# Kernel optimization log

Measured on AMD Instinct MI355X. Metric: run time of the kernel, lower is better.

Reference implementation:

```python
import jax, jax.numpy as jnp
import numpy as np

EPS = 1e-4
SLOPE = 0.01
NFFT = 512
HOP = 256
CH_IN = 8
CH_H = 64
FREQ = NFFT // 2 + 1
LEN = 48000
BATCH = 2


def hann(n):
    return (0.5 - 0.5 * jnp.cos(2.0 * np.pi * jnp.arange(n) / n)).astype(jnp.float32)


def stft(x):
    # x: (B, C, L) -> (B, 2, C, F, T)  (torch.stft: center=True, reflect pad, hann window)
    pad = NFFT // 2
    xp = jnp.pad(x, ((0, 0), (0, 0), (pad, pad)), mode='reflect')
    T = 1 + x.shape[-1] // HOP
    idx = jnp.arange(T)[:, None] * HOP + jnp.arange(NFFT)[None, :]
    frames = xp[..., idx] * hann(NFFT)            # (B, C, T, NFFT)
    sp = jnp.fft.rfft(frames, axis=-1)            # (B, C, T, F)
    sp = jnp.swapaxes(sp, -1, -2)                 # (B, C, F, T)
    return jnp.stack([sp.real, sp.imag], axis=1).astype(jnp.float32)


def istft(re, im, length):
    # re, im: (B, C, F, T) -> (B, C, length) via windowed overlap-add
    sp = jnp.swapaxes(re + 1j * im, -1, -2)       # (B, C, T, F)
    win = hann(NFFT)
    frames = jnp.fft.irfft(sp, n=NFFT, axis=-1) * win
    pad = NFFT // 2
    total = length + 2 * pad
    T = frames.shape[-2]
    idx = jnp.arange(T)[:, None] * HOP + jnp.arange(NFFT)[None, :]
    out = jnp.zeros(frames.shape[:-2] + (total,), frames.dtype).at[..., idx].add(frames)
    wsum = jnp.zeros((total,), frames.dtype).at[idx].add(jnp.broadcast_to(win ** 2, (T, NFFT)))
    return (out / jnp.maximum(wsum, 1e-11))[..., pad:pad + length]


def conv2d(x, w, b, padT=0):
    y = jax.lax.conv_general_dilated(x, w, (1, 1), ((0, 0), (padT, padT)),
                                     dimension_numbers=('NCHW', 'OIHW', 'NCHW'))
    return y + b[None, :, None, None]


def cconv(x, w, b, padT=0):
    # complex conv on x: (B,2,C,F,T); w: (2,O,C,kf,kt) = [W_real, W_imag]; b: (2,O)
    r = conv2d(x[:, 0], w[0], b[0], padT) - conv2d(x[:, 1], w[1], b[1], padT)
    i = conv2d(x[:, 1], w[0], b[0], padT) + conv2d(x[:, 0], w[1], b[1], padT)
    return jnp.stack([r, i], axis=1)


def modExp(x, m=5.0):
    em = float(np.exp(m))
    return jnp.where(x > m, (x - m) * em + em, jnp.exp(jnp.minimum(x, m)))


def cExp(t):
    e = modExp(t[:, 0]) - 1.0
    return jnp.stack([e * jnp.cos(t[:, 1] - 1.0), e * jnp.sin(t[:, 1] - 1.0)], axis=1)


def snap(x):
    x = jnp.where((x >= 0) & (x < EPS), EPS, x)
    return jnp.where((x < 0) & (x > -EPS), -EPS, x)


def cLog(t):
    re = snap(t[:, 0])
    im = snap(t[:, 1])
    real = jnp.log(jnp.sqrt(im ** 2 + re ** 2 + EPS ** 2) + 1.0)
    imag = jnp.arctan(im / re)
    return jnp.stack([real, imag], axis=1)


def cMul(a, b):
    r = a[:, 0] * b[:, 0] - a[:, 1] * b[:, 1]
    i = a[:, 0] * b[:, 1] + a[:, 1] * b[:, 0]
    return jnp.stack([r, i], axis=1)


def trelu(t, tr, b):
    nr = t[:, 0] * tr[0, 0] + t[:, 1] * tr[0, 1] + b[0]
    ni = t[:, 0] * tr[1, 0] + t[:, 1] * tr[1, 1] + b[1]
    return jnp.stack([jax.nn.leaky_relu(nr, SLOPE), jax.nn.leaky_relu(ni, SLOPE)], axis=1)


def tgate(t, tr, b):
    gr = jax.nn.sigmoid(t[:, 0] * tr[0, 0] + t[:, 1] * tr[0, 1] + b[0])
    gi = jax.nn.sigmoid(t[:, 0] * tr[1, 0] + t[:, 1] * tr[1, 1] + b[1])
    return gr * gi + (1.0 - gr) * (1.0 - gi)


def perm(t):
    return jnp.transpose(t, (0, 1, 3, 2, 4))


def lrelu(x):
    return jax.nn.leaky_relu(x, SLOPE)


def forward(mix, fs_w, fs_b, fr_w, fr_b, c1r_w, c1r_b, c1i_w, c1i_b, c1_w, c1_b,
            c2r_w, c2r_b, c2i_w, c2i_b, c2_w, c2_b, a1_t, a1_b, a2_t, a2_b,
            c3r_w, c3r_b, c3i_w, c3i_b, c3_w, c3_b, c4r_w, c4r_b, c4i_w, c4i_b,
            c4_w, c4_b, a3_t, a3_b, a4_t, a4_b, f1_w, f1_b, f2_w, f2_b,
            cw_w, cw_b, fg_t, fg_b):
    ts = perm(cconv(perm(stft(mix)), fs_w, fs_b))      # (B,2,C,F,T)
    # ---- branch 1 ----
    tl = cLog(ts)
    tl = jnp.stack([conv2d(tl[:, 0], c1r_w, c1r_b), conv2d(tl[:, 1], c1r_w, c1r_b)], 1)
    tl = jnp.stack([conv2d(lrelu(tl[:, 0]), c1i_w, c1i_b), conv2d(tl[:, 1], c1i_w, c1i_b)], 1)
    tl = trelu(cExp(tl), a1_t, a1_b)
    t = cconv(tl, c1_w, c1_b)
    tl = cLog(t)
    tl = jnp.stack([conv2d(tl[:, 0], c2r_w, c2r_b, 7), conv2d(tl[:, 1], c2r_w, c2r_b, 7)], 1)[..., :-7]
    tl = jnp.stack([conv2d(lrelu(tl[:, 0]), c2i_w, c2i_b, 7), conv2d(tl[:, 1], c2i_w, c2i_b, 7)], 1)[..., :-7]
    tl = cExp(tl)
    tl1 = tl
    tc = cconv(ts, c2_w, c2_b, 7)[..., :-7]
    t = trelu(cMul(tl, tc), a2_t, a2_b)
    t = cconv(t, f1_w, f1_b)
    td1 = jnp.sum(ts - t, axis=2, keepdims=True) / ts.shape[2]
    # ---- branch 2 ----
    tl = cLog(ts)
    tl = jnp.stack([conv2d(tl[:, 0], c3r_w, c3r_b), conv2d(tl[:, 1], c3r_w, c3r_b)], 1)
    tl = jnp.stack([conv2d(lrelu(tl[:, 0]), c3i_w, c3i_b), conv2d(tl[:, 1], c3i_w, c3i_b)], 1)
    tl = trelu(cExp(tl), a3_t, a3_b)
    t = cconv(tl, c3_w, c3_b)
    tl = cLog(t)
    tl = jnp.stack([conv2d(tl[:, 0], c4r_w, c4r_b, 7), conv2d(tl[:, 1], c4r_w, c4r_b, 7)], 1)[..., :-7]
    tl = jnp.stack([conv2d(lrelu(tl[:, 0]), c4i_w, c4i_b, 7), conv2d(tl[:, 1], c4i_w, c4i_b, 7)], 1)[..., :-7]
    tl = cExp(tl)
    tc = cconv(ts, c4_w, c4_b, 7)[..., :-7]
    t = trelu(cMul(tl, tc), a4_t, a4_b)
    td2 = cconv(t, f2_w, f2_b)                         # (B,2,1,F,T)
    # ---- fuse ----
    f = cconv(jnp.concatenate([tl1, tl], axis=2), cw_w, cw_b)
    f = tgate(f, fg_t, fg_b)[:, None]                  # (B,1,1,F,T)
    td = td1 * f + td2 * (1.0 - f)
    t = perm(cconv(perm(td), fr_w, fr_b))
    return istft(t[:, 0], t[:, 1], LEN)                # (B,1,LEN)


def setup_inputs() -> dict:
    ks = iter(jax.random.split(jax.random.key(0), 64))
    def rn(shape, s=0.05):
        return s * jax.random.normal(next(ks), shape, jnp.float32)
    F, C, H = FREQ, CH_IN, CH_H
    inp = {
        'mix': jax.random.normal(next(ks), (BATCH, C, LEN), jnp.float32),
        'fs_w': rn((2, F, F, 1, 1)), 'fs_b': rn((2, F), 0.01),
        'fr_w': rn((2, F, F, 1, 1)), 'fr_b': rn((2, F), 0.01),
        'c1r_w': rn((H, C, 1, 1)), 'c1r_b': rn((H,), 0.01),
        'c1i_w': rn((H, H, 1, 1)), 'c1i_b': rn((H,), 0.01),
        'c1_w': rn((2, H, H, 1, 1)), 'c1_b': rn((2, H), 0.01),
        'c2r_w': rn((H, H, 1, 8)), 'c2r_b': rn((H,), 0.01),
        'c2i_w': rn((H, H, 1, 8)), 'c2i_b': rn((H,), 0.01),
        'c2_w': rn((2, H, C, 1, 8)), 'c2_b': rn((2, H), 0.01),
        'a1_t': rn((2, 2, H, F, 1), 0.5), 'a1_b': rn((2, H, F, 1), 0.5),
        'a2_t': rn((2, 2, H, F, 1), 0.5), 'a2_b': rn((2, H, F, 1), 0.5),
        'c3r_w': rn((H, C, 1, 1)), 'c3r_b': rn((H,), 0.01),
        'c3i_w': rn((H, H, 1, 1)), 'c3i_b': rn((H,), 0.01),
        'c3_w': rn((2, H, H, 1, 1)), 'c3_b': rn((2, H), 0.01),
        'c4r_w': rn((H, H, 1, 8)), 'c4r_b': rn((H,), 0.01),
        'c4i_w': rn((H, H, 1, 8)), 'c4i_b': rn((H,), 0.01),
        'c4_w': rn((2, H, C, 1, 8)), 'c4_b': rn((2, H), 0.01),
        'a3_t': rn((2, 2, H, F, 1), 0.5), 'a3_b': rn((2, H, F, 1), 0.5),
        'a4_t': rn((2, 2, H, F, 1), 0.5), 'a4_b': rn((2, H, F, 1), 0.5),
        'f1_w': rn((2, C, H, 1, 1)), 'f1_b': rn((2, C), 0.01),
        'f2_w': rn((2, 1, H, 1, 1)), 'f2_b': rn((2, 1), 0.01),
        'cw_w': rn((2, 1, 2 * H, 1, 1)), 'cw_b': rn((2, 1), 0.01),
        'fg_t': rn((2, 2, 1, F, 1), 0.5), 'fg_b': rn((2, 1, F, 1), 0.5),
    }
    return inp


def reference(mix, fs_w, fs_b, fr_w, fr_b, c1r_w, c1r_b, c1i_w, c1i_b, c1_w, c1_b,
              c2r_w, c2r_b, c2i_w, c2i_b, c2_w, c2_b, a1_t, a1_b, a2_t, a2_b,
              c3r_w, c3r_b, c3i_w, c3i_b, c3_w, c3_b, c4r_w, c4r_b, c4i_w, c4i_b,
              c4_w, c4_b, a3_t, a3_b, a4_t, a4_b, f1_w, f1_b, f2_w, f2_b,
              cw_w, cw_b, fg_t, fg_b):
    return forward(mix, fs_w, fs_b, fr_w, fr_b, c1r_w, c1r_b, c1i_w, c1i_b, c1_w, c1_b,
                   c2r_w, c2r_b, c2i_w, c2i_b, c2_w, c2_b, a1_t, a1_b, a2_t, a2_b,
                   c3r_w, c3r_b, c3i_w, c3i_b, c3_w, c3_b, c4r_w, c4r_b, c4i_w, c4i_b,
                   c4_w, c4_b, a3_t, a3_b, a4_t, a4_b, f1_w, f1_b, f2_w, f2_b,
                   cw_w, cw_b, fg_t, fg_b)
```

## Files before the change

### kernel.cpp

```cpp
#include <hip/hip_runtime.h>
#include <math.h>

#define DEV __device__ __forceinline__

constexpr int B_   = 2;
constexpr int C_IN = 8;
constexpr int H_   = 64;
constexpr int F_   = 257;
constexpr int T_   = 188;
constexpr int TW   = 96;
constexpr int NFFT = 512;
constexpr int HOP  = 256;
constexpr int LEN  = 48000;
constexpr int PADL = 256;
constexpr int FT   = F_ * T_;
constexpr float EPSV  = 1e-4f;
constexpr float SLOPEV = 0.01f;
constexpr float PI2 = 6.283185307179586f;

typedef __attribute__((ext_vector_type(8))) short short8;
typedef __attribute__((ext_vector_type(4))) short short4v;
typedef __attribute__((ext_vector_type(4))) float float4v;

DEV float lrelu_f(float x) { return x > 0.f ? x : SLOPEV * x; }
DEV float snap_f(float x) {
  if (x >= 0.f && x < EPSV) return EPSV;
  if (x < 0.f && x > -EPSV) return -EPSV;
  return x;
}
DEV float modexp_f(float x) {
  const float em = 148.4131591025766f;
  return x > 5.f ? (x - 5.f) * em + em : expf(x);
}
DEV void cexp_f(float tr, float ti, float& er, float& ei) {
  float e = modexp_f(tr) - 1.f;
  float s, c;
  sincosf(ti - 1.f, &s, &c);
  er = e * c; ei = e * s;
}
DEV float sigmoid_f(float x) { return 1.f / (1.f + expf(-x)); }

DEV short f2bf(float x) {
  unsigned u = __float_as_uint(x);
  unsigned r = (u + 0x7fffu + ((u >> 16) & 1u)) >> 16;
  return (short)r;
}
DEV float bf2f(short h) {
  return __uint_as_float(((unsigned)(unsigned short)h) << 16);
}

__global__ void k_mixsplit(const float* __restrict__ x, short* __restrict__ hi,
                           short* __restrict__ lo) {
  int i = blockIdx.x * 256 + threadIdx.x;
  if (i >= B_ * C_IN * LEN / 4) return;
  float4v v = *(const float4v*)(x + (size_t)i * 4);
  short4v h, l;
  #pragma unroll
  for (int j = 0; j < 4; ++j) {
    h[j] = f2bf(v[j]);
    l[j] = f2bf(v[j] - bf2f(h[j]));
  }
  *(short4v*)(hi + (size_t)i * 4) = h;
  *(short4v*)(lo + (size_t)i * 4) = l;
}

__global__ __launch_bounds__(256) void k_mixdft(const float* __restrict__ W,
                                                short* __restrict__ wpk) {
  constexpr int MT = 33;
  __shared__ float wr_s[F_], wi_s[F_];
  int m = blockIdx.x;
  int k = blockIdx.y * 256 + threadIdx.x;
  int po = m >= F_;
  int fo = m - po * F_;
  if (m < 2 * F_) {
    for (int i = threadIdx.x; i < F_; i += 256) {
      wr_s[i] = W[fo * F_ + i];
      wi_s[i] = W[F_ * F_ + fo * F_ + i];
    }
  }
  __syncthreads();
  float val = 0.f;
  if (m < 2 * F_) {
    float sd, cd;
    sincosf((PI2 / NFFT) * k, &sd, &cd);
    float cs = 1.f, sn = 0.f;
    float ar = 0.f, ai = 0.f;
    for (int fi = 0; fi < F_; ++fi) {
      float wrv = wr_s[fi], wiv = wi_s[fi];
      ar += wrv * cs + wiv * sn;
      ai += wiv * cs - wrv * sn;
      float t2 = cs * cd - sn * sd;
      sn = sn * cd + cs * sd;
      cs = t2;
    }
    float win = 0.5f - 0.5f * cd;
    val = (po ? ai : ar) * win;
  }
  int mtg = m >> 4;
  int lane2 = ((k >> 3) & 3) * 16 + (m & 15);
  int s = k >> 5;
  int j = k & 7;
  short hi = f2bf(val);
  short lo = f2bf(val - bf2f(hi));
  wpk[(((0 * 16 + s) * MT + mtg) * 64 + lane2) * 8 + j] = hi;
  wpk[(((16 + s) * MT + mtg) * 64 + lane2) * 8 + j] = lo;
}

__global__ __launch_bounds__(256) void k_stftmix(
    const short* __restrict__ mhi, const short* __restrict__ mlo,
    const short* __restrict__ wpk, const float* __restrict__ bias,
    float* __restrict__ Y) {
  constexpr int PITCH = 136;
  constexpr int MT = 33;
  __shared__ short xs_hi[TW * PITCH];
  __shared__ short xs_lo[TW * PITCH];
  int mg = blockIdx.x;
  int bc = blockIdx.y;
  int b = bc >> 3, c = bc & 7;
  int t0 = blockIdx.z * TW;
  int tid = threadIdx.x;
  int lane = tid & 63;
  int wv = __builtin_amdgcn_readfirstlane(tid >> 6);
  int mh = wv >> 1;
  int tc = wv & 1;
  int q = lane >> 4;
  int n = lane & 15;
  int wbase = tc * 48;

  const short* mh_ = mhi + (size_t)(b * C_IN + c) * LEN;
  const short* ml_ = mlo + (size_t)(b * C_IN + c) * LEN;

  float4v acc[2][3];
  #pragma unroll
  for (int mt = 0; mt < 2; ++mt)
    #pragma unroll
    for (int nt = 0; nt < 3; ++nt) acc[mt][nt] = (float4v)(0.f);

  const short8* wp = (const short8*)wpk;
  for (int round = 0; round < 4; ++round) {
    if (round) __syncthreads();
    for (int i = tid; i < TW * 16; i += 256) {
      int tl = i >> 4, u = i & 15;
      int kk0 = u * 8;
      int t = t0 + tl;
      int g0 = t * HOP + round * 128 + kk0 - PADL;
      short8 h, l;
      if (t < T_ && g0 >= 0 && g0 + 7 < LEN) {
        h = *(const short8*)(mh_ + g0);
        l = *(const short8*)(ml_ + g0);
      } else {
        #pragma unroll
        for (int j = 0; j < 8; ++j) {
          short hv = 0, lv = 0;
          if (t < T_) {
            int g = g0 + j;
            if (g < 0) g = -g;
            if (g >= LEN) g = 2 * LEN - 2 - g;
            hv = mh_[g]; lv = ml_[g];
          }
          h[j] = hv; l[j] = lv;
        }
      }
      *(short8*)&xs_hi[tl * PITCH + kk0] = h;
      *(short8*)&xs_lo[tl * PITCH + kk0] = l;
    }
    __syncthreads();
    #pragma unroll
    for (int s2 = 0; s2 < 4; ++s2) {
      int s = round * 4 + s2;
      short8 Bh[3], Bl[3];
      #pragma unroll
      for (int nt = 0; nt < 3; ++nt) {
        int off = (wbase + nt * 16 + n) * PITCH + s2 * 32 + q * 8;
        Bh[nt] = *(const short8*)&xs_hi[off];
        Bl[nt] = *(const short8*)&xs_lo[off];
      }
      #pragma unroll
      for (int mt = 0; mt < 2; ++mt) {
        int mtg = mg * 4 + mh * 2 + mt;
        if (mtg >= MT) continue;
        short8 Ah = wp[((0 * 16 + s) * MT + mtg) * 64 + lane];
        short8 Al = wp[((16 + s) * MT + mtg) * 64 + lane];
        #pragma unroll
        for (int nt = 0; nt < 3; ++nt) {
          acc[mt][nt] = __builtin_amdgcn_mfma_f32_16x16x32_bf16(Ah, Bh[nt], acc[mt][nt], 0, 0, 0);
          acc[mt][nt] = __builtin_amdgcn_mfma_f32_16x16x32_bf16(Ah, Bl[nt], acc[mt][nt], 0, 0, 0);
          acc[mt][nt] = __builtin_amdgcn_mfma_f32_16x16x32_bf16(Al, Bh[nt], acc[mt][nt], 0, 0, 0);
        }
      }
    }
  }

  #pragma unroll
  for (int nt = 0; nt < 3; ++nt) {
    int t = t0 + wbase + nt * 16 + n;
    if (t >= T_) continue;
    #pragma unroll
    for (int mt = 0; mt < 2; ++mt) {
      int mtg = mg * 4 + mh * 2 + mt;
      if (mtg >= MT) continue;
      #pragma unroll
      for (int r = 0; r < 4; ++r) {
        int m = mtg * 16 + q * 4 + r;
        if (m >= 2 * F_) continue;
        int po = m >= F_;
        int fo = m - po * F_;
        float badd = po ? bias[fo] + bias[F_ + fo] : bias[fo] - bias[F_ + fo];
        Y[((size_t)((b * 2 + po) * C_IN + c)) * FT + fo * T_ + t] = acc[mt][nt][r] + badd;
      }
    }
  }
}

template<int CH>
__global__ void k_fmix(const float* __restrict__ X, const float* __restrict__ W,
                       const float* __restrict__ bias, float* __restrict__ Y) {
  int fo = blockIdx.x;
  int bc = blockIdx.y; int c = bc % CH; int b = bc / CH;
  int t = threadIdx.x;
  if (t >= T_) return;
  const float* wr = W + fo * F_;
  const float* wi = W + F_ * F_ + fo * F_;
  const float* xr = X + ((b * 2 + 0) * CH + c) * FT + t;
  const float* xi = X + ((b * 2 + 1) * CH + c) * FT + t;
  float ar = 0.f, ai = 0.f;
  for (int fi = 0; fi < F_; ++fi) {
    float wrv = wr[fi], wiv = wi[fi];
    float xrv = xr[fi * T_], xiv = xi[fi * T_];
    ar += wrv * xrv - wiv * xiv;
    ai += wrv * xiv + wiv * xrv;
  }
  float br = bias[fo], bi = bias[F_ + fo];
  Y[((b * 2 + 0) * CH + c) * FT + fo * T_ + t] = ar + br - bi;
  Y[((b * 2 + 1) * CH + c) * FT + fo * T_ + t] = ai + br + bi;
}

template<int CIN, int K>
DEV void repack_real_body(const float* __restrict__ W, short* __restrict__ wpk, int i) {
  constexpr int CC = (CIN >= 32) ? (CIN / 32) : 1;
  constexpr int NSTEP = (CIN * K + 31) / 32;
  int total = 2 * NSTEP * 4 * 64 * 8;
  if (i >= total) return;
  int j = i & 7;
  int lane = (i >> 3) & 63;
  int mt = (i >> 9) & 3;
  int s = (i >> 11) % NSTEP;
  int split = i / (NSTEP * 2048);
  int q = lane >> 4;
  int m = mt * 16 + (lane & 15);
  int tap = s / CC;
  int c = (s % CC) * 32 + q * 8 + j;
  float w = 0.f;
  if (c < CIN && tap < K) w = W[(m * CIN + c) * K + tap];
  short hi = f2bf(w);
  wpk[i] = split ? f2bf(w - bf2f(hi)) : hi;
}

template<int CIN2, int COUT2, int K>
DEV void repack_cplx_body(const float* __restrict__ W, short* __restrict__ wpk, int i) {
  constexpr int CIN = CIN2 / 2, COUT = COUT2 / 2;
  constexpr int NSTEP = CIN2 * K / 32;
  constexpr int MT = (COUT2 + 15) / 16;
  int total = 2 * NSTEP * MT * 64 * 8;
  if (i >= total) return;
  int j = i & 7;
  int lane = (i >> 3) & 63;
  int idx = i >> 9;
  int mt = idx % MT; idx /= MT;
  int s = idx % NSTEP;
  int split = idx / NSTEP;
  int q = lane >> 4;
  int m = mt * 16 + (lane & 15);
  int tap, pi, ci;
  if constexpr (CIN2 == 128) {
    tap = 0;
    int cs = s * 32 + q * 8 + j;
    int half = cs / 64, r = cs % 64;
    ci = half * 32 + r / 2;
    pi = r & 1;
  } else {
    tap = s * 2 + (q >> 1);
    int cs = (q & 1) * 8 + j;
    pi = cs / CIN;
    ci = cs % CIN;
  }
  float w = 0.f;
  if (m < COUT2) {
    int po = m / COUT, ho = m % COUT;
    float wr = W[((0 * COUT + ho) * CIN + ci) * K + tap];
    float wi = W[((1 * COUT + ho) * CIN + ci) * K + tap];
    w = (po == pi) ? wr : (po == 0 ? -wi : wi);
  }
  short hi = f2bf(w);
  wpk[i] = split ? f2bf(w - bf2f(hi)) : hi;
}

__global__ __launch_bounds__(256) void k_repack_all(
    const float* c1r_w, const float* c1i_w, const float* c2r_w, const float* c2i_w,
    const float* c3r_w, const float* c3i_w, const float* c4r_w, const float* c4i_w,
    const float* c1_w, const float* c2_w, const float* c3_w, const float* c4_w,
    const float* f1_w, const float* f2_w,
    short* o0, short* o1, short* o2, short* o3, short* o4, short* o5, short* o6,
    short* o7, short* o8, short* o9, short* o10, short* o11, short* o12, short* o13) {
  int i = blockIdx.x * 256 + threadIdx.x;
  switch (blockIdx.y) {
    case 0:  repack_real_body<C_IN, 1>(c1r_w, o0, i); break;
    case 1:  repack_real_body<H_,   1>(c1i_w, o1, i); break;
    case 2:  repack_real_body<H_,   8>(c2r_w, o2, i); break;
    case 3:  repack_real_body<H_,   8>(c2i_w, o3, i); break;
    case 4:  repack_real_body<C_IN, 1>(c3r_w, o4, i); break;
    case 5:  repack_real_body<H_,   1>(c3i_w, o5, i); break;
    case 6:  repack_real_body<H_,   8>(c4r_w, o6, i); break;
    case 7:  repack_real_body<H_,   8>(c4i_w, o7, i); break;
    case 8:  repack_cplx_body<128, 128, 1>(c1_w, o8, i); break;
    case 9:  repack_cplx_body<16,  128, 8>(c2_w, o9, i); break;
    case 10: repack_cplx_body<128, 128, 1>(c3_w, o10, i); break;
    case 11: repack_cplx_body<16,  128, 8>(c4_w, o11, i); break;
    case 12: repack_cplx_body<128, 16,  1>(f1_w, o12, i); break;
    case 13: repack_cplx_body<128, 2,   1>(f2_w, o13, i); break;
  }
}

template<int CIN, int K, int PRO>
__global__ __launch_bounds__(256) void k_conv_mfma(
    const float* __restrict__ X, const short* __restrict__ wpk,
    const float* __restrict__ bias, float* __restrict__ Y) {
  constexpr int CC = (CIN >= 32) ? (CIN / 32) : 1;
  constexpr int NSTEP = (CIN * K + 31) / 32;
  constexpr int PITCH = 72;
  constexpr int ROWS = TW + (K - 1);
  __shared__ short xs_hi[ROWS * PITCH];
  __shared__ short xs_lo[ROWS * PITCH];
  int f = blockIdx.x;
  int bp = blockIdx.y; int p = bp & 1; int b = bp >> 1;
  int t0 = blockIdx.z * TW;
  int tid = threadIdx.x;

  for (int i = tid; i < ROWS * PITCH; i += 256) { xs_hi[i] = 0; xs_lo[i] = 0; }
  __syncthreads();

  const float* Xr_ = X + (size_t)((b * 2 + 0) * CIN) * FT + f * T_;
  const float* Xi_ = X + (size_t)((b * 2 + 1) * CIN) * FT + f * T_;
  const float* Xp  = X + (size_t)((b * 2 + p) * CIN) * FT + f * T_;
  for (int i = tid; i < CIN * ROWS; i += 256) {
    int c = i / ROWS, rr = i % ROWS;
    int t = t0 + rr - (K - 1);
    if (t < 0 || t >= T_) continue;
    float v;
    if (PRO == 2) {
      float re = snap_f(Xr_[c * FT + t]);
      float im = snap_f(Xi_[c * FT + t]);
      v = (p == 0) ? logf(sqrtf(im * im + re * re + EPSV * EPSV) + 1.f)
                   : atanf(im / re);
    } else {
      v = Xp[c * FT + t];
      if (PRO == 1 && p == 0) v = lrelu_f(v);
    }
    short hi = f2bf(v);
    short lo = f2bf(v - bf2f(hi));
    xs_hi[rr * PITCH + c] = hi;
    xs_lo[rr * PITCH + c] = lo;
  }
  __syncthreads();

  int lane = tid & 63;
  int wv = __builtin_amdgcn_readfirstlane(tid >> 6);
  int mh = wv >> 1;
  int tc = wv & 1;
  int q = lane >> 4;
  int n = lane & 15;
  int wbase = tc * 48;

  float4v acc[2][3];
  #pragma unroll
  for (int mt = 0; mt < 2; ++mt)
    #pragma unroll
    for (int nt = 0; nt < 3; ++nt) acc[mt][nt] = (float4v)(0.f);

  const short8* wp = (const short8*)wpk;
  for (int s = 0; s < NSTEP; ++s) {
    int tap = s / CC;
    int c0 = (s % CC) * 32;
    short8 Bh[3], Bl[3];
    #pragma unroll
    for (int nt = 0; nt < 3; ++nt) {
      int off = (wbase + nt * 16 + n + tap) * PITCH + c0 + q * 8;
      Bh[nt] = *(const short8*)&xs_hi[off];
      Bl[nt] = *(const short8*)&xs_lo[off];
    }
    #pragma unroll
    for (int mt = 0; mt < 2; ++mt) {
      int mtg = mh * 2 + mt;
      short8 Ah = wp[((0 * NSTEP + s) * 4 + mtg) * 64 + lane];
      short8 Al = wp[((1 * NSTEP + s) * 4 + mtg) * 64 + lane];
      #pragma unroll
      for (int nt = 0; nt < 3; ++nt) {
        acc[mt][nt] = __builtin_amdgcn_mfma_f32_16x16x32_bf16(Ah, Bh[nt], acc[mt][nt], 0, 0, 0);
        acc[mt][nt] = __builtin_amdgcn_mfma_f32_16x16x32_bf16(Ah, Bl[nt], acc[mt][nt], 0, 0, 0);
        acc[mt][nt] = __builtin_amdgcn_mfma_f32_16x16x32_bf16(Al, Bh[nt], acc[mt][nt], 0, 0, 0);
      }
    }
  }

  float* Yp = Y + (size_t)((b * 2 + p) * H_) * FT + f * T_;
  #pragma unroll
  for (int nt = 0; nt < 3; ++nt) {
    int t = t0 + wbase + nt * 16 + n;
    if (t >= T_) continue;
    #pragma unroll
    for (int mt = 0; mt < 2; ++mt) {
      #pragma unroll
      for (int r = 0; r < 4; ++r) {
        int h = (mh * 2 + mt) * 16 + q * 4 + r;
        Yp[h * FT + t] = acc[mt][nt][r] + bias[h];
      }
    }
  }
}

template<int COUT2, int PRO>
__global__ __launch_bounds__(256) void k_cconv128(
    const float* __restrict__ X0, const float* __restrict__ X1,
    const short* __restrict__ wpk,
    const float* __restrict__ at, const float* __restrict__ ab,
    const float* __restrict__ bias, float* __restrict__ Y) {
  constexpr int MT = (COUT2 + 15) / 16;
  constexpr int MTW = (MT > 4) ? 4 : MT;
  constexpr int COUT = COUT2 / 2;
  constexpr int NSTEP = 4;
  constexpr int PITCH = 72;
  __shared__ short xs_hi[TW * PITCH];
  __shared__ short xs_lo[TW * PITCH];
  __shared__ float coef[6][64];
  int f = blockIdx.x;
  int b = blockIdx.y;
  int t0 = blockIdx.z * TW;
  int tid = threadIdx.x;
  int lane = tid & 63;
  int wv = __builtin_amdgcn_readfirstlane(tid >> 6);
  int mh = wv >> 1;
  int tc = wv & 1;
  int q = lane >> 4;
  int n = lane & 15;
  int wbase = tc * 48;

  if (tid < 64) {
    int h = tid;
    coef[0][h] = at[(0 * H_ + h) * F_ + f];
    coef[1][h] = at[(1 * H_ + h) * F_ + f];
    coef[2][h] = at[(2 * H_ + h) * F_ + f];
    coef[3][h] = at[(3 * H_ + h) * F_ + f];
    coef[4][h] = ab[h * F_ + f];
    coef[5][h] = ab[(H_ + h) * F_ + f];
  }
  for (int i = tid; i < TW * PITCH; i += 256) { xs_hi[i] = 0; xs_lo[i] = 0; }

  const float* b0r = X0 + (size_t)((b * 2 + 0) * H_) * FT + f * T_;
  const float* b0i = X0 + (size_t)((b * 2 + 1) * H_) * FT + f * T_;
  const float* b1r = X1 + (size_t)((b * 2 + 0) * H_) * FT + f * T_;
  const float* b1i = X1 + (size_t)((b * 2 + 1) * H_) * FT + f * T_;

  float4v acc[MTW][3];
  #pragma unroll
  for (int mt = 0; mt < MTW; ++mt)
    #pragma unroll
    for (int nt = 0; nt < 3; ++nt) acc[mt][nt] = (float4v)(0.f);

  const short8* wp = (const short8*)wpk;
  for (int half = 0; half < 2; ++half) {
    __syncthreads();
    for (int i = tid; i < 32 * TW; i += 256) {
      int hh = i / TW, tl = i % TW;
      int t = t0 + tl;
      if (t >= T_) continue;
      int h = half * 32 + hh;
      float xr = b0r[h * FT + t], xi = b0i[h * FT + t];
      float vr, vi;
      if (PRO == 1) {
        float er, ei;
        cexp_f(xr, xi, er, ei);
        vr = lrelu_f(er * coef[0][h] + ei * coef[1][h] + coef[4][h]);
        vi = lrelu_f(er * coef[2][h] + ei * coef[3][h] + coef[5][h]);
      } else {
        float yr = b1r[h * FT + t], yi = b1i[h * FT + t];
        float mr = xr * yr - xi * yi;
        float mi = xr * yi + xi * yr;
        vr = lrelu_f(mr * coef[0][h] + mi * coef[1][h] + coef[4][h]);
        vi = lrelu_f(mr * coef[2][h] + mi * coef[3][h] + coef[5][h]);
      }
      int cs0 = hh * 2, cs1 = hh * 2 + 1;
      short hr = f2bf(vr), hi2 = f2bf(vi);
      xs_hi[tl * PITCH + cs0] = hr;
      xs_lo[tl * PITCH + cs0] = f2bf(vr - bf2f(hr));
      xs_hi[tl * PITCH + cs1] = hi2;
      xs_lo[tl * PITCH + cs1] = f2bf(vi - bf2f(hi2));
    }
    __syncthreads();
    #pragma unroll
    for (int s2 = 0; s2 < 2; ++s2) {
      int s = half * 2 + s2;
      short8 Bh[3], Bl[3];
      #pragma unroll
      for (int nt = 0; nt < 3; ++nt) {
        int off = (wbase + nt * 16 + n) * PITCH + s2 * 32 + q * 8;
        Bh[nt] = *(const short8*)&xs_hi[off];
        Bl[nt] = *(const short8*)&xs_lo[off];
      }
      #pragma unroll
      for (int mt = 0; mt < MTW; ++mt) {
        int mtg = mh * 4 + mt;
        if (mtg >= MT) continue;
        short8 Ah = wp[((0 * NSTEP + s) * MT + mtg) * 64 + lane];
        short8 Al = wp[((1 * NSTEP + s) * MT + mtg) * 64 + lane];
        #pragma unroll
        for (int nt = 0; nt < 3; ++nt) {
          acc[mt][nt] = __builtin_amdgcn_mfma_f32_16x16x32_bf16(Ah, Bh[nt], acc[mt][nt], 0, 0, 0);
          acc[mt][nt] = __builtin_amdgcn_mfma_f32_16x16x32_bf16(Ah, Bl[nt], acc[mt][nt], 0, 0, 0);
          acc[mt][nt] = __builtin_amdgcn_mfma_f32_16x16x32_bf16(Al, Bh[nt], acc[mt][nt], 0, 0, 0);
        }
      }
    }
  }

  float* Yp = Y + (size_t)b * COUT2 * FT + f * T_;
  #pragma unroll
  for (int nt = 0; nt < 3; ++nt) {
    int t = t0 + wbase + nt * 16 + n;
    if (t >= T_) continue;
    #pragma unroll
    for (int mt = 0; mt < MTW; ++mt) {
      int mtg = mh * 4 + mt;
      if (mtg >= MT) continue;
      #pragma unroll
      for (int r = 0; r < 4; ++r) {
        int o2 = mtg * 16 + q * 4 + r;
        if (o2 >= COUT2) continue;
        int po = o2 / COUT, ho = o2 % COUT;
        float br = bias[ho], bi = bias[COUT + ho];
        float badd = (po == 0) ? br - bi : br + bi;
        Yp[o2 * FT + t] = acc[mt][nt][r] + badd;
      }
    }
  }
}

__global__ __launch_bounds__(256) void k_cconv16(
    const float* __restrict__ X, const short* __restrict__ wpk,
    const float* __restrict__ bias, float* __restrict__ Y) {
  constexpr int MT = 8, NSTEP = 4, PITCH = 24, ROWS = TW + 7, COUT = 64, COUT2 = 128;
  __shared__ short xs_hi[ROWS * PITCH];
  __shared__ short xs_lo[ROWS * PITCH];
  int f = blockIdx.x;
  int b = blockIdx.y;
  int t0 = blockIdx.z * TW;
  int tid = threadIdx.x;

  for (int i = tid; i < ROWS * PITCH; i += 256) { xs_hi[i] = 0; xs_lo[i] = 0; }
  __syncthreads();

  const float* Xp = X + (size_t)b * 16 * FT + f * T_;
  for (int i = tid; i < 16 * ROWS; i += 256) {
    int c = i / ROWS, rr = i % ROWS;
    int t = t0 + rr - 7;
    if (t < 0 || t >= T_) continue;
    float v = Xp[c * FT + t];
    short hi = f2bf(v);
    short lo = f2bf(v - bf2f(hi));
    xs_hi[rr * PITCH + c] = hi;
    xs_lo[rr * PITCH + c] = lo;
  }
  __syncthreads();

  int lane = tid & 63;
  int wv = __builtin_amdgcn_readfirstlane(tid >> 6);
  int mh = wv >> 1;
  int tc = wv & 1;
  int q = lane >> 4;
  int n = lane & 15;
  int wbase = tc * 48;

  float4v acc[4][3];
  #pragma unroll
  for (int mt = 0; mt < 4; ++mt)
    #pragma unroll
    for (int nt = 0; nt < 3; ++nt) acc[mt][nt] = (float4v)(0.f);

  const short8* wp = (const short8*)wpk;
  #pragma unroll
  for (int s = 0; s < NSTEP; ++s) {
    int tap = s * 2 + (q >> 1);
    int coff = (q & 1) * 8;
    short8 Bh[3], Bl[3];
    #pragma unroll
    for (int nt = 0; nt < 3; ++nt) {
      int off = (wbase + nt * 16 + n + tap) * PITCH + coff;
      Bh[nt] = *(const short8*)&xs_hi[off];
      Bl[nt] = *(const short8*)&xs_lo[off];
    }
    #pragma unroll
    for (int mt = 0; mt < 4; ++mt) {
      int mtg = mh * 4 + mt;
      short8 Ah = wp[((0 * NSTEP + s) * MT + mtg) * 64 + lane];
      short8 Al = wp[((1 * NSTEP + s) * MT + mtg) * 64 + lane];
      #pragma unroll
      for (int nt = 0; nt < 3; ++nt) {
        acc[mt][nt] = __builtin_amdgcn_mfma_f32_16x16x32_bf16(Ah, Bh[nt], acc[mt][nt], 0, 0, 0);
        acc[mt][nt] = __builtin_amdgcn_mfma_f32_16x16x32_bf16(Ah, Bl[nt], acc[mt][nt], 0, 0, 0);
        acc[mt][nt] = __builtin_amdgcn_mfma_f32_16x16x32_bf16(Al, Bh[nt], acc[mt][nt], 0, 0, 0);
      }
    }
  }

  float* Yp = Y + (size_t)b * COUT2 * FT + f * T_;
  #pragma unroll
  for (int nt = 0; nt < 3; ++nt) {
    int t = t0 + wbase + nt * 16 + n;
    if (t >= T_) continue;
    #pragma unroll
    for (int mt = 0; mt < 4; ++mt) {
      #pragma unroll
      for (int r = 0; r < 4; ++r) {
        int o2 = (mh * 4 + mt) * 16 + q * 4 + r;
        int po = o2 / COUT, ho = o2 % COUT;
        float br = bias[ho], bi = bias[COUT + ho];
        float badd = (po == 0) ? br - bi : br + bi;
        Yp[o2 * FT + t] = acc[mt][nt][r] + badd;
      }
    }
  }
}

__global__ void k_cexp(const float* __restrict__ X, float* __restrict__ Y) {
  int i = blockIdx.x * blockDim.x + threadIdx.x;
  if (i >= B_ * H_ * FT) return;
  int b = i / (H_ * FT);
  int r = i % (H_ * FT);
  int i0 = (b * 2) * H_ * FT + r;
  int i1 = i0 + H_ * FT;
  float er, ei;
  cexp_f(X[i0], X[i1], er, ei);
  Y[i0] = er;
  Y[i1] = ei;
}

__global__ void k_td1(const float* __restrict__ ts, const float* __restrict__ t8,
                      float* __restrict__ td1) {
  int i = blockIdx.x * blockDim.x + threadIdx.x;
  if (i >= B_ * 2 * FT) return;
  int bp = i / FT; int r = i % FT;
  const float* a = ts + bp * C_IN * FT + r;
  const float* c2 = t8 + bp * C_IN * FT + r;
  float acc = 0.f;
  #pragma unroll
  for (int c = 0; c < C_IN; ++c) acc += a[c * FT] - c2[c * FT];
  td1[i] = acc * (1.f / C_IN);
}

__global__ void k_fuse(const float* __restrict__ tl1, const float* __restrict__ tl2,
                       const float* __restrict__ td1, const float* __restrict__ td2,
                       const float* __restrict__ cw, const float* __restrict__ cwb,
                       const float* __restrict__ fgt, const float* __restrict__ fgb,
                       float* __restrict__ td) {
  int i = blockIdx.x * blockDim.x + threadIdx.x;
  if (i >= B_ * FT) return;
  int b = i / FT; int r = i % FT; int f = r / T_;
  const float* x1r = tl1 + (b * 2) * H_ * FT + r;
  const float* x1i = x1r + H_ * FT;
  const float* x2r = tl2 + (b * 2) * H_ * FT + r;
  const float* x2i = x2r + H_ * FT;
  float fr = 0.f, fi = 0.f;
  for (int c = 0; c < H_; ++c) {
    float w1r = cw[c], w2r = cw[H_ + c], w1i = cw[2 * H_ + c], w2i = cw[3 * H_ + c];
    float a1r = x1r[c * FT], a1i = x1i[c * FT];
    float a2r = x2r[c * FT], a2i = x2i[c * FT];
    fr += w1r * a1r - w1i * a1i + w2r * a2r - w2i * a2i;
    fi += w1r * a1i + w1i * a1r + w2r * a2i + w2i * a2r;
  }
  fr += cwb[0] - cwb[1];
  fi += cwb[0] + cwb[1];
  float t00 = fgt[f], t01 = fgt[F_ + f], t10 = fgt[2 * F_ + f], t11 = fgt[3 * F_ + f];
  float gr = sigmoid_f(fr * t00 + fi * t01 + fgb[f]);
  float gi = sigmoid_f(fr * t10 + fi * t11 + fgb[F_ + f]);
  float gg = gr * gi + (1.f - gr) * (1.f - gi);
  int i0 = (b * 2) * FT + r, i1 = i0 + FT;
  td[i0] = td1[i0] * gg + td2[i0] * (1.f - gg);
  td[i1] = td1[i1] * gg + td2[i1] * (1.f - gg);
}

__global__ __launch_bounds__(320) void k_iframes(const float* __restrict__ sp,
                                                 float* __restrict__ frames) {
  __shared__ float Xr[F_], Xi[F_];
  int blk = blockIdx.x;
  int t = blk % T_;
  int b = blk / T_;
  int tid = threadIdx.x;
  for (int i = tid; i < F_; i += 320) {
    Xr[i] = sp[(b * 2 + 0) * FT + i * T_ + t];
    Xi[i] = sp[(b * 2 + 1) * FT + i * T_ + t];
  }
  __syncthreads();
  int n = tid;
  if (n <= 256) {
    float sd, cd;
    sincosf((PI2 / NFFT) * n, &sd, &cd);
    float cs = cd, sn = sd;
    float ac = 0.f, as = 0.f;
    for (int f = 1; f < 256; ++f) {
      ac += Xr[f] * cs;
      as += Xi[f] * sn;
      float t2 = cs * cd - sn * sd;
      sn = sn * cd + cs * sd;
      cs = t2;
    }
    float base = Xr[0] + Xr[256] * (1.f - 2.f * (n & 1));
    float win = 0.5f - 0.5f * cd;
    float scale = win * (1.f / NFFT);
    float* fr = frames + (size_t)(b * T_ + t) * NFFT;
    fr[n] = (base + 2.f * ac - 2.f * as) * scale;
    if (n >= 1 && n <= 255)
      fr[NFFT - n] = (base + 2.f * ac + 2.f * as) * scale;
  }
}

__global__ void k_ola(const float* __restrict__ frames, float* __restrict__ out) {
  int i = blockIdx.x * blockDim.x + threadIdx.x;
  if (i >= B_ * LEN) return;
  int b = i / LEN; int j = i % LEN;
  int p = j + PADL;
  int t0 = p / HOP; int n0 = p - t0 * HOP;
  float acc = 0.f, wsum = 0.f;
  if (t0 < T_) {
    acc += frames[(b * T_ + t0) * NFFT + n0];
    float w = 0.5f - 0.5f * cosf((PI2 / NFFT) * n0);
    wsum += w * w;
  }
  int t1 = t0 - 1, n1 = n0 + HOP;
  if (t1 >= 0 && t1 < T_) {
    acc += frames[(b * T_ + t1) * NFFT + n1];
    float w = 0.5f - 0.5f * cosf((PI2 / NFFT) * n1);
    wsum += w * w;
  }
  out[i] = acc / fmaxf(wsum, 1e-11f);
}

extern "C" void kernel_launch(void* const* d_in, const int* in_sizes, int n_in,
                              void* d_out, int out_size, void* d_ws, size_t ws_size,
                              hipStream_t stream) {
  const float* mix   = (const float*)d_in[0];
  const float* fs_w  = (const float*)d_in[1];
  const float* fs_b  = (const float*)d_in[2];
  const float* fr_w  = (const float*)d_in[3];
  const float* fr_b  = (const float*)d_in[4];
  const float* c1r_w = (const float*)d_in[5];
  const float* c1r_b = (const float*)d_in[6];
  const float* c1i_w = (const float*)d_in[7];
  const float* c1i_b = (const float*)d_in[8];
  const float* c1_w  = (const float*)d_in[9];
  const float* c1_b  = (const float*)d_in[10];
  const float* c2r_w = (const float*)d_in[11];
  const float* c2r_b = (const float*)d_in[12];
  const float* c2i_w = (const float*)d_in[13];
  const float* c2i_b = (const float*)d_in[14];
  const float* c2_w  = (const float*)d_in[15];
  const float* c2_b  = (const float*)d_in[16];
  const float* a1_t  = (const float*)d_in[17];
  const float* a1_b  = (const float*)d_in[18];
  const float* a2_t  = (const float*)d_in[19];
  const float* a2_b  = (const float*)d_in[20];
  const float* c3r_w = (const float*)d_in[21];
  const float* c3r_b = (const float*)d_in[22];
  const float* c3i_w = (const float*)d_in[23];
  const float* c3i_b = (const float*)d_in[24];
  const float* c3_w  = (const float*)d_in[25];
  const float* c3_b  = (const float*)d_in[26];
  const float* c4r_w = (const float*)d_in[27];
  const float* c4r_b = (const float*)d_in[28];
  const float* c4i_w = (const float*)d_in[29];
  const float* c4i_b = (const float*)d_in[30];
  const float* c4_w  = (const float*)d_in[31];
  const float* c4_b  = (const float*)d_in[32];
  const float* a3_t  = (const float*)d_in[33];
  const float* a3_b  = (const float*)d_in[34];
  const float* a4_t  = (const float*)d_in[35];
  const float* a4_b  = (const float*)d_in[36];
  const float* f1_w  = (const float*)d_in[37];
  const float* f1_b  = (const float*)d_in[38];
  const float* f2_w  = (const float*)d_in[39];
  const float* f2_b  = (const float*)d_in[40];
  const float* cw_w  = (const float*)d_in[41];
  const float* cw_b  = (const float*)d_in[42];
  const float* fg_t  = (const float*)d_in[43];
  const float* fg_b  = (const float*)d_in[44];

  const size_t S8 = (size_t)B_ * 2 * C_IN * FT;
  const size_t SH = (size_t)B_ * 2 * H_ * FT;
  const size_t S1 = (size_t)B_ * 2 * FT;
  float* ws  = (float*)d_ws;
  float* ts0 = ws;
  float* ts  = ts0 + S8;
  float* A   = ts + S8;
  float* Bb  = A + SH;
  float* Cc  = Bb + SH;
  float* td1 = Cc + SH;
  float* td2 = td1 + S1;
  float* tdf = td2 + S1;
  float* tdr = tdf + S1;
  float* s8  = ts0;
  float* frames = ts0;

  short* wtail = (short*)(tdr + S1);
  constexpr int SZ_C8K1   = 2 * 1  * 4 * 64 * 8;
  constexpr int SZ_C64K1  = 2 * 2  * 4 * 64 * 8;
  constexpr int SZ_C64K8  = 2 * 16 * 4 * 64 * 8;
  constexpr int SZ_CC128  = 2 * 4  * 8 * 64 * 8;
  constexpr int SZ_CF     = 2 * 4  * 1 * 64 * 8;
  constexpr int SZ_SM     = 2 * 16 * 33 * 64 * 8;
  short* w_c1r = wtail;
  short* w_c1i = w_c1r + SZ_C8K1;
  short* w_c2r = w_c1i + SZ_C64K1;
  short* w_c2i = w_c2r + SZ_C64K8;
  short* w_c3r = w_c2i + SZ_C64K8;
  short* w_c3i = w_c3r + SZ_C8K1;
  short* w_c4r = w_c3i + SZ_C64K1;
  short* w_c4i = w_c4r + SZ_C64K8;
  short* w_cc1 = w_c4i + SZ_C64K8;
  short* w_cc2 = w_cc1 + SZ_CC128;
  short* w_cc3 = w_cc2 + SZ_CC128;
  short* w_cc4 = w_cc3 + SZ_CC128;
  short* w_cf1 = w_cc4 + SZ_CC128;
  short* w_cf2 = w_cf1 + SZ_CF;
  short* w_sm  = w_cf2 + SZ_CF;
  short* mhi   = w_sm + SZ_SM;
  short* mlo   = mhi + (size_t)B_ * C_IN * LEN;

  const int nH = B_ * H_ * FT;
  const int nP = B_ * FT;
  const dim3 rgrid(F_, B_ * 2, 2);
  const dim3 cgrid(F_, B_, 2);

  k_repack_all<<<dim3(256, 14), 256, 0, stream>>>(
      c1r_w, c1i_w, c2r_w, c2i_w, c3r_w, c3i_w, c4r_w, c4i_w,
      c1_w, c2_w, c3_w, c4_w, f1_w, f2_w,
      w_c1r, w_c1i, w_c2r, w_c2i, w_c3r, w_c3i, w_c4r, w_c4i,
      w_cc1, w_cc2, w_cc3, w_cc4, w_cf1, w_cf2);

  k_mixsplit<<<(B_ * C_IN * LEN / 4 + 255) / 256, 256, 0, stream>>>(mix, mhi, mlo);
  k_mixdft<<<dim3(528, 2), 256, 0, stream>>>(fs_w, w_sm);
  k_stftmix<<<dim3(9, 16, 2), 256, 0, stream>>>(mhi, mlo, w_sm, fs_b, ts);

  k_conv_mfma<C_IN, 1, 2><<<rgrid, 256, 0, stream>>>(ts, w_c1r, c1r_b, A);
  k_conv_mfma<H_, 1, 1><<<rgrid, 256, 0, stream>>>(A, w_c1i, c1i_b, Bb);
  k_cconv128<128, 1><<<cgrid, 256, 0, stream>>>(Bb, Bb, w_cc1, a1_t, a1_b, c1_b, A);
  k_conv_mfma<H_, 8, 2><<<rgrid, 256, 0, stream>>>(A, w_c2r, c2r_b, Bb);
  k_conv_mfma<H_, 8, 1><<<rgrid, 256, 0, stream>>>(Bb, w_c2i, c2i_b, A);
  k_cexp<<<(nH + 255) / 256, 256, 0, stream>>>(A, Bb);
  k_cconv16<<<cgrid, 256, 0, stream>>>(ts, w_cc2, c2_b, A);
  k_cconv128<16, 2><<<cgrid, 256, 0, stream>>>(Bb, A, w_cf1, a2_t, a2_b, f1_b, s8);
  k_td1<<<(B_ * 2 * FT + 255) / 256, 256, 0, stream>>>(ts, s8, td1);

  k_conv_mfma<C_IN, 1, 2><<<rgrid, 256, 0, stream>>>(ts, w_c3r, c3r_b, A);
  k_conv_mfma<H_, 1, 1><<<rgrid, 256, 0, stream>>>(A, w_c3i, c3i_b, Cc);
  k_cconv128<128, 1><<<cgrid, 256, 0, stream>>>(Cc, Cc, w_cc3, a3_t, a3_b, c3_b, A);
  k_conv_mfma<H_, 8, 2><<<rgrid, 256, 0, stream>>>(A, w_c4r, c4r_b, Cc);
  k_conv_mfma<H_, 8, 1><<<rgrid, 256, 0, stream>>>(Cc, w_c4i, c4i_b, A);
  k_cexp<<<(nH + 255) / 256, 256, 0, stream>>>(A, Cc);
  k_cconv16<<<cgrid, 256, 0, stream>>>(ts, w_cc4, c4_b, A);
  k_cconv128<2, 2><<<cgrid, 256, 0, stream>>>(Cc, A, w_cf2, a4_t, a4_b, f2_b, td2);

  k_fuse<<<(nP + 255) / 256, 256, 0, stream>>>(Bb, Cc, td1, td2, cw_w, cw_b, fg_t, fg_b, tdf);
  k_fmix<1><<<dim3(F_, B_), 192, 0, stream>>>(tdf, fr_w, fr_b, tdr);
  k_iframes<<<B_ * T_, 320, 0, stream>>>(tdr, frames);
  k_ola<<<(B_ * LEN + 255) / 256, 256, 0, stream>>>(frames, (float*)d_out);
}
```

Measured before the change: 864.4 us.

## Use fast intrinsics, retile STFT-mix kernel, and hoist conv weight loads

Replaces expf/sincosf/logf/atanf/cosf with hardware intrinsics and a polynomial atan, cutting transcendental cost in several elementwise paths. The STFT-mix kernel now tiles 48 time frames per block, with one M tile per wave, and launches twice as many blocks to improve occupancy and cut LDS. The conv kernel fully unrolls its step loop and hoists the A-fragment loads ahead of the B loads. The fast math lowers accuracy, and the polynomial atan has an error near 1e-5 that may matter against tolerance.

```diff
diff --git a/kernel.cpp b/kernel.cpp
--- a/kernel.cpp
+++ b/kernel.cpp
@@ -28,17 +28,30 @@
   if (x < 0.f && x > -EPSV) return -EPSV;
   return x;
 }
+DEV float fast_atan(float z) {
+  float az = fabsf(z);
+  float u = az > 1.f ? __builtin_amdgcn_rcpf(az) : az;
+  float u2 = u * u;
+  float p = -0.01172120f;
+  p = p * u2 + 0.05265332f;
+  p = p * u2 - 0.11643287f;
+  p = p * u2 + 0.19354346f;
+  p = p * u2 - 0.33262347f;
+  p = p * u2 + 0.99997726f;
+  float r = p * u;
+  if (az > 1.f) r = 1.5707963267948966f - r;
+  return z < 0.f ? -r : r;
+}
 DEV float modexp_f(float x) {
   const float em = 148.4131591025766f;
-  return x > 5.f ? (x - 5.f) * em + em : expf(x);
+  return x > 5.f ? (x - 5.f) * em + em : __expf(x);
 }
 DEV void cexp_f(float tr, float ti, float& er, float& ei) {
   float e = modexp_f(tr) - 1.f;
-  float s, c;
-  sincosf(ti - 1.f, &s, &c);
-  er = e * c; ei = e * s;
-}
-DEV float sigmoid_f(float x) { return 1.f / (1.f + expf(-x)); }
+  float a = ti - 1.f;
+  er = e * __cosf(a); ei = e * __sinf(a);
+}
+DEV float sigmoid_f(float x) { return 1.f / (1.f + __expf(-x)); }
 
 DEV short f2bf(float x) {
   unsigned u = __float_as_uint(x);
@@ -106,40 +119,37 @@
   wpk[(((16 + s) * MT + mtg) * 64 + lane2) * 8 + j] = lo;
 }
 
+constexpr int TWS = 48;
 __global__ __launch_bounds__(256) void k_stftmix(
     const short* __restrict__ mhi, const short* __restrict__ mlo,
     const short* __restrict__ wpk, const float* __restrict__ bias,
     float* __restrict__ Y) {
   constexpr int PITCH = 136;
   constexpr int MT = 33;
-  __shared__ short xs_hi[TW * PITCH];
-  __shared__ short xs_lo[TW * PITCH];
+  __shared__ short xs_hi[TWS * PITCH];
+  __shared__ short xs_lo[TWS * PITCH];
   int mg = blockIdx.x;
   int bc = blockIdx.y;
   int b = bc >> 3, c = bc & 7;
-  int t0 = blockIdx.z * TW;
+  int t0 = blockIdx.z * TWS;
   int tid = threadIdx.x;
   int lane = tid & 63;
   int wv = __builtin_amdgcn_readfirstlane(tid >> 6);
-  int mh = wv >> 1;
-  int tc = wv & 1;
+  int mtg = mg * 4 + wv;
   int q = lane >> 4;
   int n = lane & 15;
-  int wbase = tc * 48;
 
   const short* mh_ = mhi + (size_t)(b * C_IN + c) * LEN;
   const short* ml_ = mlo + (size_t)(b * C_IN + c) * LEN;
 
-  float4v acc[2][3];
-  #pragma unroll
-  for (int mt = 0; mt < 2; ++mt)
-    #pragma unroll
-    for (int nt = 0; nt < 3; ++nt) acc[mt][nt] = (float4v)(0.f);
+  float4v acc[3];
+  #pragma unroll
+  for (int nt = 0; nt < 3; ++nt) acc[nt] = (float4v)(0.f);
 
   const short8* wp = (const short8*)wpk;
   for (int round = 0; round < 4; ++round) {
     if (round) __syncthreads();
-    for (int i = tid; i < TW * 16; i += 256) {
+    for (int i = tid; i < TWS * 16; i += 256) {
       int tl = i >> 4, u = i & 15;
       int kk0 = u * 8;
       int t = t0 + tl;
@@ -168,37 +178,34 @@
     #pragma unroll
     for (int s2 = 0; s2 < 4; ++s2) {
       int s = round * 4 + s2;
+      short8 Ah, Al;
+      if (mtg < MT) {
+        Ah = wp[((0 * 16 + s) * MT + mtg) * 64 + lane];
+        Al = wp[((16 + s) * MT + mtg) * 64 + lane];
+      }
       short8 Bh[3], Bl[3];
       #pragma unroll
       for (int nt = 0; nt < 3; ++nt) {
-        int off = (wbase + nt * 16 + n) * PITCH + s2 * 32 + q * 8;
+        int off = (nt * 16 + n) * PITCH + s2 * 32 + q * 8;
         Bh[nt] = *(const short8*)&xs_hi[off];
         Bl[nt] = *(const short8*)&xs_lo[off];
       }
-      #pragma unroll
-      for (int mt = 0; mt < 2; ++mt) {
-        int mtg = mg * 4 + mh * 2 + mt;
-        if (mtg >= MT) continue;
-        short8 Ah = wp[((0 * 16 + s) * MT + mtg) * 64 + lane];
-        short8 Al = wp[((16 + s) * MT + mtg) * 64 + lane];
+      if (mtg < MT) {
         #pragma unroll
         for (int nt = 0; nt < 3; ++nt) {
-          acc[mt][nt] = __builtin_amdgcn_mfma_f32_16x16x32_bf16(Ah, Bh[nt], acc[mt][nt], 0, 0, 0);
-          acc[mt][nt] = __builtin_amdgcn_mfma_f32_16x16x32_bf16(Ah, Bl[nt], acc[mt][nt], 0, 0, 0);
-          acc[mt][nt] = __builtin_amdgcn_mfma_f32_16x16x32_bf16(Al, Bh[nt], acc[mt][nt], 0, 0, 0);
+          acc[nt] = __builtin_amdgcn_mfma_f32_16x16x32_bf16(Ah, Bh[nt], acc[nt], 0, 0, 0);
+          acc[nt] = __builtin_amdgcn_mfma_f32_16x16x32_bf16(Ah, Bl[nt], acc[nt], 0, 0, 0);
+          acc[nt] = __builtin_amdgcn_mfma_f32_16x16x32_bf16(Al, Bh[nt], acc[nt], 0, 0, 0);
         }
       }
     }
   }
 
-  #pragma unroll
-  for (int nt = 0; nt < 3; ++nt) {
-    int t = t0 + wbase + nt * 16 + n;
-    if (t >= T_) continue;
-    #pragma unroll
-    for (int mt = 0; mt < 2; ++mt) {
-      int mtg = mg * 4 + mh * 2 + mt;
-      if (mtg >= MT) continue;
+  if (mtg < MT) {
+    #pragma unroll
+    for (int nt = 0; nt < 3; ++nt) {
+      int t = t0 + nt * 16 + n;
+      if (t >= T_) continue;
       #pragma unroll
       for (int r = 0; r < 4; ++r) {
         int m = mtg * 16 + q * 4 + r;
@@ -206,7 +213,7 @@
         int po = m >= F_;
         int fo = m - po * F_;
         float badd = po ? bias[fo] + bias[F_ + fo] : bias[fo] - bias[F_ + fo];
-        Y[((size_t)((b * 2 + po) * C_IN + c)) * FT + fo * T_ + t] = acc[mt][nt][r] + badd;
+        Y[((size_t)((b * 2 + po) * C_IN + c)) * FT + fo * T_ + t] = acc[nt][r] + badd;
       }
     }
   }
@@ -350,8 +357,8 @@
     if (PRO == 2) {
       float re = snap_f(Xr_[c * FT + t]);
       float im = snap_f(Xi_[c * FT + t]);
-      v = (p == 0) ? logf(sqrtf(im * im + re * re + EPSV * EPSV) + 1.f)
-                   : atanf(im / re);
+      v = (p == 0) ? __logf(sqrtf(im * im + re * re + EPSV * EPSV) + 1.f)
+                   : fast_atan(im / re);
     } else {
       v = Xp[c * FT + t];
       if (PRO == 1 && p == 0) v = lrelu_f(v);
@@ -378,9 +385,17 @@
     for (int nt = 0; nt < 3; ++nt) acc[mt][nt] = (float4v)(0.f);
 
   const short8* wp = (const short8*)wpk;
+  #pragma unroll
   for (int s = 0; s < NSTEP; ++s) {
     int tap = s / CC;
     int c0 = (s % CC) * 32;
+    short8 Ah[2], Al[2];
+    #pragma unroll
+    for (int mt = 0; mt < 2; ++mt) {
+      int mtg = mh * 2 + mt;
+      Ah[mt] = wp[((0 * NSTEP + s) * 4 + mtg) * 64 + lane];
+      Al[mt] = wp[((1 * NSTEP + s) * 4 + mtg) * 64 + lane];
+    }
     short8 Bh[3], Bl[3];
     #pragma unroll
     for (int nt = 0; nt < 3; ++nt) {
@@ -390,14 +405,11 @@
     }
     #pragma unroll
     for (int mt = 0; mt < 2; ++mt) {
-      int mtg = mh * 2 + mt;
-      short8 Ah = wp[((0 * NSTEP + s) * 4 + mtg) * 64 + lane];
-      short8 Al = wp[((1 * NSTEP + s) * 4 + mtg) * 64 + lane];
       #pragma unroll
       for (int nt = 0; nt < 3; ++nt) {
-        acc[mt][nt] = __builtin_amdgcn_mfma_f32_16x16x32_bf16(Ah, Bh[nt], acc[mt][nt], 0, 0, 0);
-        acc[mt][nt] = __builtin_amdgcn_mfma_f32_16x16x32_bf16(Ah, Bl[nt], acc[mt][nt], 0, 0, 0);
-        acc[mt][nt] = __builtin_amdgcn_mfma_f32_16x16x32_bf16(Al, Bh[nt], acc[mt][nt], 0, 0, 0);
+        acc[mt][nt] = __builtin_amdgcn_mfma_f32_16x16x32_bf16(Ah[mt], Bh[nt], acc[mt][nt], 0, 0, 0);
+        acc[mt][nt] = __builtin_amdgcn_mfma_f32_16x16x32_bf16(Ah[mt], Bl[nt], acc[mt][nt], 0, 0, 0);
+        acc[mt][nt] = __builtin_amdgcn_mfma_f32_16x16x32_bf16(Al[mt], Bh[nt], acc[mt][nt], 0, 0, 0);
       }
     }
   }
@@ -731,13 +743,13 @@
   float acc = 0.f, wsum = 0.f;
   if (t0 < T_) {
     acc += frames[(b * T_ + t0) * NFFT + n0];
-    float w = 0.5f - 0.5f * cosf((PI2 / NFFT) * n0);
+    float w = 0.5f - 0.5f * __cosf((PI2 / NFFT) * n0);
     wsum += w * w;
   }
   int t1 = t0 - 1, n1 = n0 + HOP;
   if (t1 >= 0 && t1 < T_) {
     acc += frames[(b * T_ + t1) * NFFT + n1];
-    float w = 0.5f - 0.5f * cosf((PI2 / NFFT) * n1);
+    float w = 0.5f - 0.5f * __cosf((PI2 / NFFT) * n1);
     wsum += w * w;
   }
   out[i] = acc / fmaxf(wsum, 1e-11f);
@@ -846,7 +858,7 @@
 
   k_mixsplit<<<(B_ * C_IN * LEN / 4 + 255) / 256, 256, 0, stream>>>(mix, mhi, mlo);
   k_mixdft<<<dim3(528, 2), 256, 0, stream>>>(fs_w, w_sm);
-  k_stftmix<<<dim3(9, 16, 2), 256, 0, stream>>>(mhi, mlo, w_sm, fs_b, ts);
+  k_stftmix<<<dim3(9, 16, 4), 256, 0, stream>>>(mhi, mlo, w_sm, fs_b, ts);
 
   k_conv_mfma<C_IN, 1, 2><<<rgrid, 256, 0, stream>>>(ts, w_c1r, c1r_b, A);
   k_conv_mfma<H_, 1, 1><<<rgrid, 256, 0, stream>>>(A, w_c1i, c1i_b, Bb);
```

Result: faster. 846.1 us (-2.1%).
